# Optimization experiments

Hardware: AMD Instinct MI355X
Metric: run time of the kernel (lower is better)

## Reference

```python
import jax, jax.numpy as jnp
import numpy as np

T, B, I, H, L = 512, 64, 1024, 1024, 2


def setup_inputs() -> dict:
    key = jax.random.key(0)
    ks = jax.random.split(key, 3)
    stdv = 1.0 / np.sqrt(H)
    x = jax.random.normal(ks[0], (T, B, I), dtype=jnp.float32)
    w_ih = jax.random.uniform(ks[1], (L, 4 * H, I), dtype=jnp.float32, minval=-stdv, maxval=stdv)
    w_hh = jax.random.uniform(ks[2], (L, 4 * H, H), dtype=jnp.float32, minval=-stdv, maxval=stdv)
    b_ih = jnp.zeros((L, 4 * H), dtype=jnp.float32)
    b_hh = jnp.zeros((L, 4 * H), dtype=jnp.float32)
    h0 = jnp.zeros((L, B, H), dtype=jnp.float32)
    c0 = jnp.zeros((L, B, H), dtype=jnp.float32)
    return {"x": x, "h0": h0, "c0": c0, "w_ih": w_ih, "w_hh": w_hh, "b_ih": b_ih, "b_hh": b_hh}


def _lstm_layer(seq, h, c, w_ih_l, w_hh_l, b_ih_l, b_hh_l):
    # in2hidden: one big GEMM over all timesteps, as in the torch code
    igates = jnp.einsum('tbi,gi->tbg', seq, w_ih_l) + b_ih_l  # (T, B, 4H)

    def step(carry, ig):
        h, c = carry
        gates = ig + h @ w_hh_l.T + b_hh_l          # (B, 4H)
        i_g, f_g, g_g, o_g = jnp.split(gates, 4, axis=-1)
        c = jax.nn.sigmoid(f_g) * c + jax.nn.sigmoid(i_g) * jnp.tanh(g_g)
        h = jax.nn.sigmoid(o_g) * jnp.tanh(c)
        return (h, c), h

    (hT, cT), out = jax.lax.scan(step, (h, c), igates)
    return out, hT, cT


def reference(x, h0, c0, w_ih, w_hh, b_ih, b_hh):
    out = x
    h_fin, c_fin = [], []
    for l in range(L):  # small fixed number of structurally distinct layers
        out, hT, cT = _lstm_layer(out, h0[l], c0[l], w_ih[l], w_hh[l], b_ih[l], b_hh[l])
        h_fin.append(hT)
        c_fin.append(cT)
    return out, jnp.stack(h_fin), jnp.stack(c_fin)
```

## Files before the change

### kernel.cpp

```cpp
#include <hip/hip_runtime.h>
#include <hip/hip_bf16.h>
#include <stdint.h>

#define T_STEPS 512
#define NBATCH 64
#define HID 1024
#define NGATE 4096
#define NLAYERS 2
#define BH (NBATCH * HID)
#define TBH (T_STEPS * NBATCH * HID)
#define WEL ((size_t)NLAYERS * NGATE * HID)
#define NBLK 256

typedef __attribute__((ext_vector_type(8))) short short8;
typedef __attribute__((ext_vector_type(4))) float f32x4;

__device__ __forceinline__ ushort f2bf(float f) {
  union { float f; uint32_t i; } u; u.f = f;
  return (ushort)((u.i + 0x7fffu + ((u.i >> 16) & 1u)) >> 16);
}

#define ISSC(S, M, OFF) \
  asm volatile("global_load_dwordx4 %0, %1, off offset:" #OFF \
               : "=v"(fr[S]) : "v"(aP[M]));
#define ISSU(S, M, OFF) \
  asm volatile("global_load_dwordx4 %0, %1, off offset:" #OFF " sc0 sc1" \
               : "=v"(fr[S]) : "v"(aP[M]));
#define VMW(N, SLOT) \
  asm volatile("s_waitcnt vmcnt(" #N ")" : "+v"(fr[SLOT]));
#define CON(S, M, KC) { \
    accA[M] = __builtin_amdgcn_mfma_f32_16x16x32_bf16(fr[S], breg[0][KC], accA[M], 0, 0, 0); \
    accB[M] = __builtin_amdgcn_mfma_f32_16x16x32_bf16(fr[S], breg[1][KC], accB[M], 0, 0, 0); }

#define PIPE(I) \
  I(0,0,0)    I(1,1,0)    I(2,2,0)    I(3,3,0)   \
  I(4,0,64)   I(5,1,64)   I(6,2,64)   I(7,3,64)  \
  I(8,0,128)  I(9,1,128)  I(10,2,128) I(11,3,128)\
  I(12,0,192) I(13,1,192) I(14,2,192) I(15,3,192)\
  VMW(15,0)  CON(0,0,0)  I(0,0,256)  \
  VMW(15,1)  CON(1,1,0)  I(1,1,256)  \
  VMW(15,2)  CON(2,2,0)  I(2,2,256)  \
  VMW(15,3)  CON(3,3,0)  I(3,3,256)  \
  VMW(15,4)  CON(4,0,1)  I(4,0,320)  \
  VMW(15,5)  CON(5,1,1)  I(5,1,320)  \
  VMW(15,6)  CON(6,2,1)  I(6,2,320)  \
  VMW(15,7)  CON(7,3,1)  I(7,3,320)  \
  VMW(15,8)  CON(8,0,2)  I(8,0,384)  \
  VMW(15,9)  CON(9,1,2)  I(9,1,384)  \
  VMW(15,10) CON(10,2,2) I(10,2,384) \
  VMW(15,11) CON(11,3,2) I(11,3,384) \
  VMW(15,12) CON(12,0,3) I(12,0,448) \
  VMW(15,13) CON(13,1,3) I(13,1,448) \
  VMW(15,14) CON(14,2,3) I(14,2,448) \
  VMW(15,15) CON(15,3,3) I(15,3,448) \
  VMW(15,0)  CON(0,0,4)  \
  VMW(14,1)  CON(1,1,4)  \
  VMW(13,2)  CON(2,2,4)  \
  VMW(12,3)  CON(3,3,4)  \
  VMW(11,4)  CON(4,0,5)  \
  VMW(10,5)  CON(5,1,5)  \
  VMW(9,6)   CON(6,2,5)  \
  VMW(8,7)   CON(7,3,5)  \
  VMW(7,8)   CON(8,0,6)  \
  VMW(6,9)   CON(9,1,6)  \
  VMW(5,10)  CON(10,2,6) \
  VMW(4,11)  CON(11,3,6) \
  VMW(3,12)  CON(12,0,7) \
  VMW(2,13)  CON(13,1,7) \
  VMW(1,14)  CON(14,2,7) \
  VMW(0,15)  CON(15,3,7)

__global__ void k_f32_to_bf16(const float* __restrict__ in, ushort* __restrict__ out, int n) {
  int i = (blockIdx.x * blockDim.x + threadIdx.x) * 4;
  if (i >= n) return;
  const float4 v = *reinterpret_cast<const float4*>(in + i);
  ushort4 o; o.x = f2bf(v.x); o.y = f2bf(v.y); o.z = f2bf(v.z); o.w = f2bf(v.w);
  *reinterpret_cast<ushort4*>(out + i) = o;
}
__global__ void k_zero(int* p, int n) {
  int i = blockIdx.x * blockDim.x + threadIdx.x;
  if (i < n) p[i] = 0;
}

struct ScanP {
  const ushort* wih; const ushort* whh;
  const ushort* xb;  const ushort* hinit;
  ushort* h0r;
  ushort* h1d;
  const float* c0; const float* bi; const float* bh;
  float* out; int* bar;
};

__device__ __forceinline__ void gbar(int* bar, int phase, int stripe, bool isRoot) {
  __syncthreads();
  if (threadIdx.x == 0) {
    __hip_atomic_fetch_add(bar + stripe * 16, 1, __ATOMIC_RELAXED, __HIP_MEMORY_SCOPE_AGENT);
    if (isRoot) {
      const int target = (phase + 1) * NBLK;
      for (;;) {
        int sum = 0;
#pragma unroll
        for (int i = 0; i < 16; ++i)
          sum += __hip_atomic_load(bar + i * 16, __ATOMIC_RELAXED, __HIP_MEMORY_SCOPE_AGENT);
        if (sum >= target) break;
        __builtin_amdgcn_s_sleep(1);
      }
      __hip_atomic_store(bar + 256, phase + 1, __ATOMIC_RELAXED, __HIP_MEMORY_SCOPE_AGENT);
    } else {
      while (__hip_atomic_load(bar + 256, __ATOMIC_RELAXED, __HIP_MEMORY_SCOPE_AGENT) < phase + 1)
        __builtin_amdgcn_s_sleep(2);
    }
  }
  __syncthreads();
  __builtin_amdgcn_sched_barrier(0);
}

__global__ __launch_bounds__(512, 2) void k_scan(ScanP p) {
  __shared__ float glds[8][32][100];
  const int tid = threadIdx.x, wave = tid >> 6, lane = tid & 63;
  const bool isL1 = blockIdx.x >= 128;
  const int cb = isL1 ? (int)blockIdx.x - 128 : (int)blockIdx.x;
  const int j0 = cb * 8;
  const int stripe = blockIdx.x & 15;
  const bool isRoot = (blockIdx.x == 0);
  const bool hiSrc = wave >= 4;
  const int koff = (wave & 3) * 256;

  const ushort* wihL = p.wih + (isL1 ? (size_t)NGATE * HID : 0);
  const ushort* whhL = p.whh + (isL1 ? (size_t)NGATE * HID : 0);
  const ushort* bsrc = hiSrc ? whhL : wihL;
  short8 breg[2][8];
#pragma unroll
  for (int t = 0; t < 2; ++t) {
    const int i = t * 16 + (lane & 15);
    const int g = (i >> 3) * 1024 + j0 + (i & 7);
    const ushort* bp = bsrc + (size_t)g * 1024 + koff + (lane >> 4) * 8;
#pragma unroll
    for (int kc = 0; kc < 8; ++kc) breg[t][kc] = *(const short8*)(bp + kc * 32);
  }

  const int eb = tid >> 3, jl = tid & 7, jj = j0 + jl;
  const int lofs = isL1 ? NGATE : 0;
  float creg = p.c0[(isL1 ? BH : 0) + eb * 1024 + jj];
  float bias[4];
#pragma unroll
  for (int g = 0; g < 4; ++g)
    bias[g] = p.bi[lofs + g * 1024 + jj] + p.bh[lofs + g * 1024 + jj];

  const size_t arow = (size_t)(lane & 15) * 1024 + koff + (lane >> 4) * 8;

  for (int s = 0; s < T_STEPS + 1; ++s) {
    const bool act = isL1 ? (s >= 1) : (s < T_STEPS);
    if (act) {
      const ushort* src;
      if (!isL1) src = hiSrc ? ((s == 0) ? p.hinit : p.h0r + (size_t)(s - 1) * BH)
                             : (p.xb + (size_t)s * BH);
      else       src = hiSrc ? ((s == 1) ? p.hinit + BH : p.h1d + (size_t)(s & 1) * BH)
                             : (p.h0r + (size_t)(s - 1) * BH);
      const ushort* base = src + arow;
      const ushort* aP[4] = { base, base + 16 * 1024, base + 32 * 1024, base + 48 * 1024 };
      f32x4 accA[4], accB[4];
#pragma unroll
      for (int m = 0; m < 4; ++m) {
        accA[m] = (f32x4){0.f, 0.f, 0.f, 0.f};
        accB[m] = (f32x4){0.f, 0.f, 0.f, 0.f};
      }
      short8 fr[16];
      if (isL1 && hiSrc) { PIPE(ISSU) } else { PIPE(ISSC) }

      {
        const int r0 = lane & 15, q4 = (lane >> 4) * 4;
#pragma unroll
        for (int m = 0; m < 4; ++m) {
          *(f32x4*)&glds[wave][r0][m * 16 + q4]      = accA[m];
          *(f32x4*)&glds[wave][16 + r0][m * 16 + q4] = accB[m];
        }
      }
      __syncthreads();

      float v[4];
#pragma unroll
      for (int g = 0; g < 4; ++g) {
        float t = bias[g];
#pragma unroll
        for (int w = 0; w < 8; ++w) t += glds[w][g * 8 + jl][eb];
        v[g] = t;
      }
      float c = creg;
      const float si = 1.f / (1.f + __expf(-v[0]));
      const float sf = 1.f / (1.f + __expf(-v[1]));
      const float tg = tanhf(v[2]);
      const float so = 1.f / (1.f + __expf(-v[3]));
      c = sf * c + si * tg;
      const float h = so * tanhf(c);
      creg = c;

      const uint32_t hu = (uint32_t)f2bf(h);
      const uint32_t other = __shfl_xor(hu, 1);
      ushort* hdst = (!isL1) ? (p.h0r + (size_t)s * BH)
                             : (p.h1d + (size_t)((s - 1) & 1) * BH);
      if (!(tid & 1)) {
        uint32_t* hw = (uint32_t*)(hdst + eb * 1024 + jj);
        const uint32_t packed = hu | (other << 16);
        __hip_atomic_store(hw, packed, __ATOMIC_RELAXED, __HIP_MEMORY_SCOPE_AGENT);
        uint32_t chk = __hip_atomic_load(hw, __ATOMIC_RELAXED, __HIP_MEMORY_SCOPE_AGENT);
        asm volatile("" :: "v"(chk));
      }

      if (isL1) {
        p.out[(size_t)(s - 1) * BH + eb * 1024 + jj] = h;
        if (s - 1 == T_STEPS - 1) {
          p.out[(size_t)TBH + BH + eb * 1024 + jj] = h;
          p.out[(size_t)TBH + 3 * BH + eb * 1024 + jj] = c;
        }
      } else if (s == T_STEPS - 1) {
        p.out[(size_t)TBH + eb * 1024 + jj] = h;
        p.out[(size_t)TBH + 2 * BH + eb * 1024 + jj] = c;
      }
    }
    gbar(p.bar, s, stripe, isRoot);
  }
}

extern "C" void kernel_launch(void* const* d_in, const int* in_sizes, int n_in,
                              void* d_out, int out_size, void* d_ws, size_t ws_size,
                              hipStream_t stream) {
  const float* x    = (const float*)d_in[0];
  const float* h0   = (const float*)d_in[1];
  const float* c0   = (const float*)d_in[2];
  const float* w_ih = (const float*)d_in[3];
  const float* w_hh = (const float*)d_in[4];
  const float* b_ih = (const float*)d_in[5];
  const float* b_hh = (const float*)d_in[6];
  float* out = (float*)d_out;

  ushort* xb    = (ushort*)d_ws;
  ushort* wihb  = xb + (size_t)TBH;
  ushort* whhb  = wihb + WEL;
  ushort* hinit = whhb + WEL;
  ushort* h0r   = hinit + 2 * (size_t)BH;
  ushort* h1d   = h0r + (size_t)TBH;
  int*    bar   = (int*)(h1d + 2 * (size_t)BH);

  const size_t need = ((size_t)2 * TBH + 2 * WEL + 4 * (size_t)BH) * 2 + 4096;
  if (ws_size < need) return;

  { int n = TBH;        k_f32_to_bf16<<<(n / 4 + 255) / 256, 256, 0, stream>>>(x, xb, n); }
  { int n = (int)WEL;   k_f32_to_bf16<<<(n / 4 + 255) / 256, 256, 0, stream>>>(w_ih, wihb, n); }
  { int n = (int)WEL;   k_f32_to_bf16<<<(n / 4 + 255) / 256, 256, 0, stream>>>(w_hh, whhb, n); }
  { int n = 2 * BH;     k_f32_to_bf16<<<(n / 4 + 255) / 256, 256, 0, stream>>>(h0, hinit, n); }
  k_zero<<<2, 256, 0, stream>>>(bar, 512);

  ScanP sp;
  sp.wih = wihb; sp.whh = whhb;
  sp.xb = xb; sp.hinit = hinit;
  sp.h0r = h0r; sp.h1d = h1d;
  sp.c0 = c0; sp.bi = b_ih; sp.bh = b_hh;
  sp.out = out; sp.bar = bar;

  void* kp[1] = {&sp};
  hipLaunchCooperativeKernel(reinterpret_cast<void*>(&k_scan),
                             dim3(NBLK), dim3(512), kp, 0, stream);
}
```

Measured before the change: 6.880 ms.

## Decouple layer barriers and stage weights in LDS with 32x32 MFMA tiles

Replaces the single grid-wide barrier over both layers with two per-layer barriers plus release counters, so layer 1 waits only on layer 0's step-t release and its own previous step. This lets the layers run as a wavefront pipeline rather than in lockstep. Weights now sit in LDS (128KB per block), loaded via global_load_lds, instead of registers, and the MFMA shape moves from 16x16x32 to 32x32x16 with a K-split reduction tree through shared memory. Layer 1's hidden history is kept for every timestep, not double-buffered, which removes the uncached-load path but uses more workspace. The extra __syncthreads reduction stages and large LDS footprint may limit occupancy or add per-step latency.

```diff
diff --git a/kernel.cpp b/kernel.cpp
--- a/kernel.cpp
+++ b/kernel.cpp
@@ -10,65 +10,65 @@
 #define BH (NBATCH * HID)
 #define TBH (T_STEPS * NBATCH * HID)
 #define WEL ((size_t)NLAYERS * NGATE * HID)
-#define NBLK 256
+#define GBLK 128
 
 typedef __attribute__((ext_vector_type(8))) short short8;
-typedef __attribute__((ext_vector_type(4))) float f32x4;
+typedef __attribute__((ext_vector_type(16))) float f32x16;
 
 __device__ __forceinline__ ushort f2bf(float f) {
   union { float f; uint32_t i; } u; u.f = f;
   return (ushort)((u.i + 0x7fffu + ((u.i >> 16) & 1u)) >> 16);
 }
-
-#define ISSC(S, M, OFF) \
+__device__ __forceinline__ void gll16(const void* g, void* l) {
+  __builtin_amdgcn_global_load_lds(
+      (const __attribute__((address_space(1))) unsigned int*)g,
+      (__attribute__((address_space(3))) unsigned int*)l, 16, 0, 0);
+}
+
+#define ISS(S, OFF) \
   asm volatile("global_load_dwordx4 %0, %1, off offset:" #OFF \
-               : "=v"(fr[S]) : "v"(aP[M]));
-#define ISSU(S, M, OFF) \
-  asm volatile("global_load_dwordx4 %0, %1, off offset:" #OFF " sc0 sc1" \
-               : "=v"(fr[S]) : "v"(aP[M]));
+               : "=v"(fr[S]) : "v"(aPtr));
 #define VMW(N, SLOT) \
   asm volatile("s_waitcnt vmcnt(" #N ")" : "+v"(fr[SLOT]));
-#define CON(S, M, KC) { \
-    accA[M] = __builtin_amdgcn_mfma_f32_16x16x32_bf16(fr[S], breg[0][KC], accA[M], 0, 0, 0); \
-    accB[M] = __builtin_amdgcn_mfma_f32_16x16x32_bf16(fr[S], breg[1][KC], accB[M], 0, 0, 0); }
-
-#define PIPE(I) \
-  I(0,0,0)    I(1,1,0)    I(2,2,0)    I(3,3,0)   \
-  I(4,0,64)   I(5,1,64)   I(6,2,64)   I(7,3,64)  \
-  I(8,0,128)  I(9,1,128)  I(10,2,128) I(11,3,128)\
-  I(12,0,192) I(13,1,192) I(14,2,192) I(15,3,192)\
-  VMW(15,0)  CON(0,0,0)  I(0,0,256)  \
-  VMW(15,1)  CON(1,1,0)  I(1,1,256)  \
-  VMW(15,2)  CON(2,2,0)  I(2,2,256)  \
-  VMW(15,3)  CON(3,3,0)  I(3,3,256)  \
-  VMW(15,4)  CON(4,0,1)  I(4,0,320)  \
-  VMW(15,5)  CON(5,1,1)  I(5,1,320)  \
-  VMW(15,6)  CON(6,2,1)  I(6,2,320)  \
-  VMW(15,7)  CON(7,3,1)  I(7,3,320)  \
-  VMW(15,8)  CON(8,0,2)  I(8,0,384)  \
-  VMW(15,9)  CON(9,1,2)  I(9,1,384)  \
-  VMW(15,10) CON(10,2,2) I(10,2,384) \
-  VMW(15,11) CON(11,3,2) I(11,3,384) \
-  VMW(15,12) CON(12,0,3) I(12,0,448) \
-  VMW(15,13) CON(13,1,3) I(13,1,448) \
-  VMW(15,14) CON(14,2,3) I(14,2,448) \
-  VMW(15,15) CON(15,3,3) I(15,3,448) \
-  VMW(15,0)  CON(0,0,4)  \
-  VMW(14,1)  CON(1,1,4)  \
-  VMW(13,2)  CON(2,2,4)  \
-  VMW(12,3)  CON(3,3,4)  \
-  VMW(11,4)  CON(4,0,5)  \
-  VMW(10,5)  CON(5,1,5)  \
-  VMW(9,6)   CON(6,2,5)  \
-  VMW(8,7)   CON(7,3,5)  \
-  VMW(7,8)   CON(8,0,6)  \
-  VMW(6,9)   CON(9,1,6)  \
-  VMW(5,10)  CON(10,2,6) \
-  VMW(4,11)  CON(11,3,6) \
-  VMW(3,12)  CON(12,0,7) \
-  VMW(2,13)  CON(13,1,7) \
-  VMW(1,14)  CON(14,2,7) \
-  VMW(0,15)  CON(15,3,7)
+#define CONS(S, KC) { \
+    const short8 bv = *(const short8*)(bB + (KC) * 1024); \
+    acc = __builtin_amdgcn_mfma_f32_32x32x16_bf16(fr[S], bv, acc, 0, 0, 0); }
+
+#define PIPE32X() \
+  ISS(0,0)   ISS(1,32)  ISS(2,64)  ISS(3,96)  ISS(4,128) ISS(5,160) ISS(6,192) ISS(7,224) \
+  ISS(8,256) ISS(9,288) ISS(10,320) ISS(11,352) ISS(12,384) ISS(13,416) ISS(14,448) ISS(15,480) \
+  VMW(15,0)  CONS(0,0)   ISS(0,512)  \
+  VMW(15,1)  CONS(1,1)   ISS(1,544)  \
+  VMW(15,2)  CONS(2,2)   ISS(2,576)  \
+  VMW(15,3)  CONS(3,3)   ISS(3,608)  \
+  VMW(15,4)  CONS(4,4)   ISS(4,640)  \
+  VMW(15,5)  CONS(5,5)   ISS(5,672)  \
+  VMW(15,6)  CONS(6,6)   ISS(6,704)  \
+  VMW(15,7)  CONS(7,7)   ISS(7,736)  \
+  VMW(15,8)  CONS(8,8)   ISS(8,768)  \
+  VMW(15,9)  CONS(9,9)   ISS(9,800)  \
+  VMW(15,10) CONS(10,10) ISS(10,832) \
+  VMW(15,11) CONS(11,11) ISS(11,864) \
+  VMW(15,12) CONS(12,12) ISS(12,896) \
+  VMW(15,13) CONS(13,13) ISS(13,928) \
+  VMW(15,14) CONS(14,14) ISS(14,960) \
+  VMW(15,15) CONS(15,15) ISS(15,992) \
+  VMW(15,0)  CONS(0,16)  \
+  VMW(14,1)  CONS(1,17)  \
+  VMW(13,2)  CONS(2,18)  \
+  VMW(12,3)  CONS(3,19)  \
+  VMW(11,4)  CONS(4,20)  \
+  VMW(10,5)  CONS(5,21)  \
+  VMW(9,6)   CONS(6,22)  \
+  VMW(8,7)   CONS(7,23)  \
+  VMW(7,8)   CONS(8,24)  \
+  VMW(6,9)   CONS(9,25)  \
+  VMW(5,10)  CONS(10,26) \
+  VMW(4,11)  CONS(11,27) \
+  VMW(3,12)  CONS(12,28) \
+  VMW(2,13)  CONS(13,29) \
+  VMW(1,14)  CONS(14,30) \
+  VMW(0,15)  CONS(15,31)
 
 __global__ void k_f32_to_bf16(const float* __restrict__ in, ushort* __restrict__ out, int n) {
   int i = (blockIdx.x * blockDim.x + threadIdx.x) * 4;
@@ -86,60 +86,53 @@
   const ushort* wih; const ushort* whh;
   const ushort* xb;  const ushort* hinit;
   ushort* h0r;
-  ushort* h1d;
+  ushort* h1r;
   const float* c0; const float* bi; const float* bh;
   float* out; int* bar;
 };
 
-__device__ __forceinline__ void gbar(int* bar, int phase, int stripe, bool isRoot) {
-  __syncthreads();
-  if (threadIdx.x == 0) {
-    __hip_atomic_fetch_add(bar + stripe * 16, 1, __ATOMIC_RELAXED, __HIP_MEMORY_SCOPE_AGENT);
-    if (isRoot) {
-      const int target = (phase + 1) * NBLK;
-      for (;;) {
-        int sum = 0;
-#pragma unroll
-        for (int i = 0; i < 16; ++i)
-          sum += __hip_atomic_load(bar + i * 16, __ATOMIC_RELAXED, __HIP_MEMORY_SCOPE_AGENT);
-        if (sum >= target) break;
-        __builtin_amdgcn_s_sleep(1);
-      }
-      __hip_atomic_store(bar + 256, phase + 1, __ATOMIC_RELAXED, __HIP_MEMORY_SCOPE_AGENT);
-    } else {
-      while (__hip_atomic_load(bar + 256, __ATOMIC_RELAXED, __HIP_MEMORY_SCOPE_AGENT) < phase + 1)
-        __builtin_amdgcn_s_sleep(2);
-    }
+__device__ __forceinline__ void wgate(const int* rel, int target, int& seen) {
+  if (seen < target) {
+    int v = __hip_atomic_load(rel, __ATOMIC_RELAXED, __HIP_MEMORY_SCOPE_AGENT);
+    while (v < target) {
+      __builtin_amdgcn_s_sleep(2);
+      v = __hip_atomic_load(rel, __ATOMIC_RELAXED, __HIP_MEMORY_SCOPE_AGENT);
+    }
+    seen = v;
+    __builtin_amdgcn_sched_barrier(0);
   }
-  __syncthreads();
-  __builtin_amdgcn_sched_barrier(0);
 }
 
 __global__ __launch_bounds__(512, 2) void k_scan(ScanP p) {
-  __shared__ float glds[8][32][100];
+  __shared__ __align__(16) ushort Wl[256 * 256];
+  __shared__ float glds[4][32][36];
   const int tid = threadIdx.x, wave = tid >> 6, lane = tid & 63;
   const bool isL1 = blockIdx.x >= 128;
   const int cb = isL1 ? (int)blockIdx.x - 128 : (int)blockIdx.x;
   const int j0 = cb * 8;
-  const int stripe = blockIdx.x & 15;
-  const bool isRoot = (blockIdx.x == 0);
-  const bool hiSrc = wave >= 4;
-  const int koff = (wave & 3) * 256;
+  const int stripe = cb & 15;
+  const bool isRoot = (cb == 0);
+  int* gb = p.bar + (isL1 ? 512 : 0);
+  const int* rel0 = p.bar + 256;
+  const int* rel1 = p.bar + 768;
+  int* relOwn = p.bar + (isL1 ? 768 : 256);
+  const int Mtile = wave >> 2, quarter = wave & 3;
 
   const ushort* wihL = p.wih + (isL1 ? (size_t)NGATE * HID : 0);
   const ushort* whhL = p.whh + (isL1 ? (size_t)NGATE * HID : 0);
-  const ushort* bsrc = hiSrc ? whhL : wihL;
-  short8 breg[2][8];
-#pragma unroll
-  for (int t = 0; t < 2; ++t) {
-    const int i = t * 16 + (lane & 15);
-    const int g = (i >> 3) * 1024 + j0 + (i & 7);
-    const ushort* bp = bsrc + (size_t)g * 1024 + koff + (lane >> 4) * 8;
-#pragma unroll
-    for (int kc = 0; kc < 8; ++kc) breg[t][kc] = *(const short8*)(bp + kc * 32);
+  {
+    const int r = lane & 31;
+    const int grow = (r >> 3) * 1024 + j0 + (r & 7);
+    for (int inst = wave; inst < 128; inst += 8) {
+      const int c0 = inst * 2;
+      const ushort* basew = (c0 < 128) ? wihL : whhL;
+      const ushort* gsrc = basew + (size_t)grow * 1024 + ((c0 & 127) + (lane >> 5)) * 8;
+      gll16(gsrc, (char*)Wl + inst * 1024);
+    }
   }
 
   const int eb = tid >> 3, jl = tid & 7, jj = j0 + jl;
+  const int tile = eb >> 5, row = eb & 31;
   const int lofs = isL1 ? NGATE : 0;
   float creg = p.c0[(isL1 ? BH : 0) + eb * 1024 + jj];
   float bias[4];
@@ -147,78 +140,116 @@
   for (int g = 0; g < 4; ++g)
     bias[g] = p.bi[lofs + g * 1024 + jj] + p.bh[lofs + g * 1024 + jj];
 
-  const size_t arow = (size_t)(lane & 15) * 1024 + koff + (lane >> 4) * 8;
-
-  for (int s = 0; s < T_STEPS + 1; ++s) {
-    const bool act = isL1 ? (s >= 1) : (s < T_STEPS);
-    if (act) {
-      const ushort* src;
-      if (!isL1) src = hiSrc ? ((s == 0) ? p.hinit : p.h0r + (size_t)(s - 1) * BH)
-                             : (p.xb + (size_t)s * BH);
-      else       src = hiSrc ? ((s == 1) ? p.hinit + BH : p.h1d + (size_t)(s & 1) * BH)
-                             : (p.h0r + (size_t)(s - 1) * BH);
-      const ushort* base = src + arow;
-      const ushort* aP[4] = { base, base + 16 * 1024, base + 32 * 1024, base + 48 * 1024 };
-      f32x4 accA[4], accB[4];
-#pragma unroll
-      for (int m = 0; m < 4; ++m) {
-        accA[m] = (f32x4){0.f, 0.f, 0.f, 0.f};
-        accB[m] = (f32x4){0.f, 0.f, 0.f, 0.f};
+  const size_t aoffE = (size_t)(Mtile * 32 + (lane & 31)) * 1024
+                     + (size_t)(quarter & 1) * 512 + (size_t)(lane >> 5) * 8;
+  const char* bB = (const char*)Wl + quarter * 32768 + (lane >> 5) * 512 + (lane & 31) * 16;
+  float* slotp = &glds[wave >> 1][0][0];
+
+  int seen0 = 0, seen1 = 0;
+
+  __syncthreads();
+
+  for (int t = 0; t < T_STEPS; ++t) {
+    const ushort* src;
+    if (!isL1) {
+      if (quarter < 2) src = p.xb + (size_t)t * BH;
+      else { if (t > 0) { wgate(relOwn, t, seen0); src = p.h0r + (size_t)(t - 1) * BH; }
+             else src = p.hinit; }
+    } else {
+      if (quarter < 2) { wgate(rel0, t + 1, seen0); src = p.h0r + (size_t)t * BH; }
+      else { if (t > 0) { wgate(relOwn, t, seen1); src = p.h1r + (size_t)(t - 1) * BH; }
+             else src = p.hinit + BH; }
+    }
+
+    f32x16 acc;
+#pragma unroll
+    for (int r = 0; r < 16; ++r) acc[r] = 0.f;
+    short8 fr[16];
+    const ushort* aPtr = src + aoffE;
+    PIPE32X()
+
+    if (wave & 1) {
+#pragma unroll
+      for (int r = 0; r < 16; ++r)
+        slotp[((r & 3) + 8 * (r >> 2) + 4 * (lane >> 5)) * 36 + (lane & 31)] = acc[r];
+    }
+    __syncthreads();
+    if (!(wave & 1)) {
+#pragma unroll
+      for (int r = 0; r < 16; ++r)
+        acc[r] += slotp[((r & 3) + 8 * (r >> 2) + 4 * (lane >> 5)) * 36 + (lane & 31)];
+    }
+    __syncthreads();
+    if (!(wave & 1) && (wave & 2)) {
+      float* s2 = &glds[wave >> 2][0][0];
+#pragma unroll
+      for (int r = 0; r < 16; ++r)
+        s2[((r & 3) + 8 * (r >> 2) + 4 * (lane >> 5)) * 36 + (lane & 31)] = acc[r];
+    }
+    __syncthreads();
+    if ((wave & 3) == 0) {
+      float* s2 = &glds[wave >> 2][0][0];
+      float* sf = &glds[2 + (wave >> 2)][0][0];
+#pragma unroll
+      for (int r = 0; r < 16; ++r) {
+        const int pr = (r & 3) + 8 * (r >> 2) + 4 * (lane >> 5);
+        sf[pr * 36 + (lane & 31)] = acc[r] + s2[pr * 36 + (lane & 31)];
       }
-      short8 fr[16];
-      if (isL1 && hiSrc) { PIPE(ISSU) } else { PIPE(ISSC) }
-
-      {
-        const int r0 = lane & 15, q4 = (lane >> 4) * 4;
-#pragma unroll
-        for (int m = 0; m < 4; ++m) {
-          *(f32x4*)&glds[wave][r0][m * 16 + q4]      = accA[m];
-          *(f32x4*)&glds[wave][16 + r0][m * 16 + q4] = accB[m];
+    }
+    __syncthreads();
+
+    const float* gfin = &glds[2 + tile][0][0];
+    const float vi = bias[0] + gfin[row * 36 + jl];
+    const float vf = bias[1] + gfin[row * 36 + 8 + jl];
+    const float vg = bias[2] + gfin[row * 36 + 16 + jl];
+    const float vo = bias[3] + gfin[row * 36 + 24 + jl];
+    float c = creg;
+    const float si = 1.f / (1.f + __expf(-vi));
+    const float sf_ = 1.f / (1.f + __expf(-vf));
+    const float tg = tanhf(vg);
+    const float so = 1.f / (1.f + __expf(-vo));
+    c = sf_ * c + si * tg;
+    const float h = so * tanhf(c);
+    creg = c;
+
+    const uint32_t hu = (uint32_t)f2bf(h);
+    const uint32_t other = __shfl_xor(hu, 1);
+    ushort* hdst = (!isL1) ? (p.h0r + (size_t)t * BH) : (p.h1r + (size_t)t * BH);
+    if (!(tid & 1)) {
+      uint32_t* hw = (uint32_t*)(hdst + eb * 1024 + jj);
+      const uint32_t packed = hu | (other << 16);
+      __hip_atomic_store(hw, packed, __ATOMIC_RELAXED, __HIP_MEMORY_SCOPE_AGENT);
+      uint32_t chk = __hip_atomic_load(hw, __ATOMIC_RELAXED, __HIP_MEMORY_SCOPE_AGENT);
+      asm volatile("" :: "v"(chk));
+    }
+
+    if (isL1) {
+      p.out[(size_t)t * BH + eb * 1024 + jj] = h;
+      if (t == T_STEPS - 1) {
+        p.out[(size_t)TBH + BH + eb * 1024 + jj] = h;
+        p.out[(size_t)TBH + 3 * BH + eb * 1024 + jj] = c;
+      }
+    } else if (t == T_STEPS - 1) {
+      p.out[(size_t)TBH + eb * 1024 + jj] = h;
+      p.out[(size_t)TBH + 2 * BH + eb * 1024 + jj] = c;
+    }
+
+    __syncthreads();
+    if (tid == 0) {
+      __hip_atomic_fetch_add(gb + stripe * 16, 1, __ATOMIC_RELAXED, __HIP_MEMORY_SCOPE_AGENT);
+      if (isRoot) {
+        const int need = (t + 1) * GBLK;
+        for (;;) {
+          int sum = 0;
+#pragma unroll
+          for (int i = 0; i < 16; ++i)
+            sum += __hip_atomic_load(gb + i * 16, __ATOMIC_RELAXED, __HIP_MEMORY_SCOPE_AGENT);
+          if (sum >= need) break;
+          __builtin_amdgcn_s_sleep(1);
         }
+        __hip_atomic_store((int*)relOwn, t + 1, __ATOMIC_RELAXED, __HIP_MEMORY_SCOPE_AGENT);
       }
-      __syncthreads();
-
-      float v[4];
-#pragma unroll
-      for (int g = 0; g < 4; ++g) {
-        float t = bias[g];
-#pragma unroll
-        for (int w = 0; w < 8; ++w) t += glds[w][g * 8 + jl][eb];
-        v[g] = t;
-      }
-      float c = creg;
-      const float si = 1.f / (1.f + __expf(-v[0]));
-      const float sf = 1.f / (1.f + __expf(-v[1]));
-      const float tg = tanhf(v[2]);
-      const float so = 1.f / (1.f + __expf(-v[3]));
-      c = sf * c + si * tg;
-      const float h = so * tanhf(c);
-      creg = c;
-
-      const uint32_t hu = (uint32_t)f2bf(h);
-      const uint32_t other = __shfl_xor(hu, 1);
-      ushort* hdst = (!isL1) ? (p.h0r + (size_t)s * BH)
-                             : (p.h1d + (size_t)((s - 1) & 1) * BH);
-      if (!(tid & 1)) {
-        uint32_t* hw = (uint32_t*)(hdst + eb * 1024 + jj);
-        const uint32_t packed = hu | (other << 16);
-        __hip_atomic_store(hw, packed, __ATOMIC_RELAXED, __HIP_MEMORY_SCOPE_AGENT);
-        uint32_t chk = __hip_atomic_load(hw, __ATOMIC_RELAXED, __HIP_MEMORY_SCOPE_AGENT);
-        asm volatile("" :: "v"(chk));
-      }
-
-      if (isL1) {
-        p.out[(size_t)(s - 1) * BH + eb * 1024 + jj] = h;
-        if (s - 1 == T_STEPS - 1) {
-          p.out[(size_t)TBH + BH + eb * 1024 + jj] = h;
-          p.out[(size_t)TBH + 3 * BH + eb * 1024 + jj] = c;
-        }
-      } else if (s == T_STEPS - 1) {
-        p.out[(size_t)TBH + eb * 1024 + jj] = h;
-        p.out[(size_t)TBH + 2 * BH + eb * 1024 + jj] = c;
-      }
-    }
-    gbar(p.bar, s, stripe, isRoot);
+    }
   }
 }
 
@@ -239,26 +270,26 @@
   ushort* whhb  = wihb + WEL;
   ushort* hinit = whhb + WEL;
   ushort* h0r   = hinit + 2 * (size_t)BH;
-  ushort* h1d   = h0r + (size_t)TBH;
-  int*    bar   = (int*)(h1d + 2 * (size_t)BH);
-
-  const size_t need = ((size_t)2 * TBH + 2 * WEL + 4 * (size_t)BH) * 2 + 4096;
+  ushort* h1r   = h0r + (size_t)TBH;
+  int*    bar   = (int*)(h1r + (size_t)TBH);
+
+  const size_t need = ((size_t)3 * TBH + 2 * WEL + 2 * (size_t)BH) * 2 + 8192;
   if (ws_size < need) return;
 
   { int n = TBH;        k_f32_to_bf16<<<(n / 4 + 255) / 256, 256, 0, stream>>>(x, xb, n); }
   { int n = (int)WEL;   k_f32_to_bf16<<<(n / 4 + 255) / 256, 256, 0, stream>>>(w_ih, wihb, n); }
   { int n = (int)WEL;   k_f32_to_bf16<<<(n / 4 + 255) / 256, 256, 0, stream>>>(w_hh, whhb, n); }
   { int n = 2 * BH;     k_f32_to_bf16<<<(n / 4 + 255) / 256, 256, 0, stream>>>(h0, hinit, n); }
-  k_zero<<<2, 256, 0, stream>>>(bar, 512);
+  k_zero<<<4, 256, 0, stream>>>(bar, 1024);
 
   ScanP sp;
   sp.wih = wihb; sp.whh = whhb;
   sp.xb = xb; sp.hinit = hinit;
-  sp.h0r = h0r; sp.h1d = h1d;
+  sp.h0r = h0r; sp.h1r = h1r;
   sp.c0 = c0; sp.bi = b_ih; sp.bh = b_hh;
   sp.out = out; sp.bar = bar;
 
   void* kp[1] = {&sp};
   hipLaunchCooperativeKernel(reinterpret_cast<void*>(&k_scan),
-                             dim3(NBLK), dim3(512), kp, 0, stream);
-}
+                             dim3(256), dim3(512), kp, 0, stream);
+}
```

Result: faster. 6.310 ms (-8.3%).
